# Kernel tuning notes

Measured on AMD Instinct MI355X. Metric: run time of the kernel, lower is better.

The kernel has to match this reference:

```python
import jax, jax.numpy as jnp
import numpy as np

N_NODES = 100000

def gin_conv(x, edge_index, W, b):
    # PyG GINConv with eps=0: out = Linear(x + sum_{j->i} x_j)
    src, dst = edge_index[0], edge_index[1]
    agg = jax.ops.segment_sum(x[src], dst, num_segments=N_NODES)  # [N, d]
    return (x + agg) @ W + b

def setup_inputs() -> dict:
    key = jax.random.key(0)
    ks = jax.random.split(key, 8)
    x = jax.random.normal(ks[0], (N_NODES, 32), dtype=jnp.float32)
    edge_index = jax.random.randint(ks[1], (2, 1600000), 0, N_NODES, dtype=jnp.int64)
    def lin(k, fan_in, fan_out):
        kw, kb = jax.random.split(k)
        lim = 1.0 / np.sqrt(fan_in)
        W = jax.random.uniform(kw, (fan_in, fan_out), minval=-lim, maxval=lim, dtype=jnp.float32)
        b = jax.random.uniform(kb, (fan_out,), minval=-lim, maxval=lim, dtype=jnp.float32)
        return W, b
    W1, b1 = lin(ks[2], 32, 64)
    W2, b2 = lin(ks[3], 64, 64)
    W3, b3 = lin(ks[4], 64, 10)
    return {"x": x, "edge_index": edge_index,
            "W1": W1, "b1": b1, "W2": W2, "b2": b2, "W3": W3, "b3": b3}

def reference(x, edge_index, W1, b1, W2, b2, W3, b3):
    h = jax.nn.relu(gin_conv(x, edge_index, W1, b1))
    h = jax.nn.relu(gin_conv(h, edge_index, W2, b2))
    return gin_conv(h, edge_index, W3, b3)  # [N, classes] logits
```

## Files before the change

### kernel.cpp

```cpp
#include <hip/hip_runtime.h>


#define GIN_N 100000
#define NBUCKET 256
#define NB2 391
#define BSTRIDE 8192
#define EPT 16

typedef float v2f __attribute__((ext_vector_type(2)));
typedef float f32x4 __attribute__((ext_vector_type(4)));
typedef short s16x8 __attribute__((ext_vector_type(8)));
typedef unsigned int u32x4 __attribute__((ext_vector_type(4)));

__device__ __forceinline__ float bf_lo(unsigned int u) {
    return __uint_as_float(u << 16);
}
__device__ __forceinline__ float bf_hi(unsigned int u) {
    return __uint_as_float(u & 0xffff0000u);
}
__device__ __forceinline__ unsigned int f2bf(float f) {
    unsigned int u = __float_as_uint(f);
    return (u + 0x7fffu + ((u >> 16) & 1u)) >> 16;
}
__device__ __forceinline__ unsigned pk2bf(float lo, float hi) {
    return f2bf(lo) | (f2bf(hi) << 16);
}
__device__ __forceinline__ v2f fp8lo(unsigned u) {
    return __builtin_amdgcn_cvt_pk_f32_fp8(u, false);
}
__device__ __forceinline__ v2f fp8hi(unsigned u) {
    return __builtin_amdgcn_cvt_pk_f32_fp8(u, true);
}
__device__ __forceinline__ s16x8 lds_frag(const unsigned* p) {
    return __builtin_bit_cast(s16x8, *reinterpret_cast<const u32x4*>(p));
}

template <int S>
__device__ __forceinline__ void blelloch_excl(int* a) {
#pragma unroll
    for (int d = 1; d < S; d <<= 1) {
        __syncthreads();
        int idx = (threadIdx.x + 1) * (d << 1) - 1;
        if (idx < S) a[idx] += a[idx - d];
    }
    __syncthreads();
    if (threadIdx.x == 0) a[S - 1] = 0;
#pragma unroll
    for (int d = S >> 1; d >= 1; d >>= 1) {
        __syncthreads();
        int idx = (threadIdx.x + 1) * (d << 1) - 1;
        if (idx < S) {
            int t = a[idx - d];
            a[idx - d] = a[idx];
            a[idx] += t;
        }
    }
    __syncthreads();
}

__global__ __launch_bounds__(256) void build_kernel(
        const int* __restrict__ src, const int* __restrict__ dst, int E,
        unsigned* __restrict__ bucketbuf, int* __restrict__ cursor,
        const float* __restrict__ x, unsigned* __restrict__ xq, int n8,
        int bblk) {
    __shared__ int h[NBUCKET];
    __shared__ int base[NBUCKET];
    int tid = threadIdx.x;
    if (blockIdx.x >= bblk) {
        int t = (blockIdx.x - bblk) * 256 + tid;
        if (t >= n8) return;
        const float4* v = reinterpret_cast<const float4*>(x);
        float4 a = v[2 * t], b = v[2 * t + 1];
        unsigned w0 = 0, w1 = 0;
        w0 = __builtin_amdgcn_cvt_pk_fp8_f32(a.x, a.y, w0, false);
        w0 = __builtin_amdgcn_cvt_pk_fp8_f32(a.z, a.w, w0, true);
        w1 = __builtin_amdgcn_cvt_pk_fp8_f32(b.x, b.y, w1, false);
        w1 = __builtin_amdgcn_cvt_pk_fp8_f32(b.z, b.w, w1, true);
        reinterpret_cast<uint2*>(xq)[t] = make_uint2(w0, w1);
        return;
    }
    int chunk0 = blockIdx.x * (256 * EPT);
    h[tid] = 0;
    __syncthreads();
    int myb[EPT];
    unsigned myrec[EPT];
#pragma unroll
    for (int i = 0; i < EPT; ++i) {
        int e = chunk0 + tid + i * 256;
        if (e < E) {
            int d = dst[e];
            int s = src[e];
            int b = d / NB2;
            myb[i] = b;
            myrec[i] = ((unsigned)(d - b * NB2) << 17) | (unsigned)s;
            atomicAdd(&h[b], 1);
        } else {
            myb[i] = -1;
        }
    }
    __syncthreads();
    base[tid] = atomicAdd(&cursor[tid], h[tid]);
    h[tid] = 0;
    __syncthreads();
#pragma unroll
    for (int i = 0; i < EPT; ++i) {
        int b = myb[i];
        if (b < 0) continue;
        int pos = base[b] + atomicAdd(&h[b], 1);
        if (pos < BSTRIDE) bucketbuf[(size_t)b * BSTRIDE + pos] = myrec[i];
    }
}

__global__ __launch_bounds__(256) void csr_build_kernel(
        const unsigned* __restrict__ bucketbuf,
        const int* __restrict__ cursor,
        int* __restrict__ rowptr,
        int* __restrict__ adj) {
    __shared__ int csr[BSTRIDE];
    __shared__ int cnt[512];
    __shared__ int off[512];
    __shared__ int bscan[NBUCKET];
    int b = blockIdx.x;
    int tid = threadIdx.x;
    bscan[tid] = cursor[tid];
    int mycnt = cursor[b];
    if (mycnt > BSTRIDE) mycnt = BSTRIDE;
    blelloch_excl<NBUCKET>(bscan);
    int base = bscan[b];

    const unsigned* buf = bucketbuf + (size_t)b * BSTRIDE;
    cnt[tid] = 0;
    cnt[tid + 256] = 0;
    __syncthreads();
    for (int i = tid; i < mycnt; i += 256)
        atomicAdd(&cnt[buf[i] >> 17], 1);
    __syncthreads();
    off[tid] = cnt[tid];
    off[tid + 256] = cnt[tid + 256];
    blelloch_excl<512>(off);

    int nodes0 = b * NB2;
    int nn2 = GIN_N + 1 - nodes0;
    if (nn2 > NB2) nn2 = NB2;
    for (int l = tid; l < nn2; l += 256) rowptr[nodes0 + l] = base + off[l];
    __syncthreads();

    for (int i = tid; i < mycnt; i += 256) {
        unsigned r = buf[i];
        int pos = atomicAdd(&off[r >> 17], 1);
        csr[pos] = (int)(r & 0x1FFFFu);
    }
    __syncthreads();
    for (int i = tid; i < mycnt; i += 256) adj[base + i] = csr[i];
}

__global__ __launch_bounds__(256, 8) void fused1_kernel(
        const float* __restrict__ xf,
        const unsigned* __restrict__ xq,
        const int* __restrict__ rowptr,
        const int* __restrict__ adj,
        const float* __restrict__ W,
        const float* __restrict__ b,
        unsigned* __restrict__ outq) {
    constexpr int K = 32, M = 64;
    constexpr int TPN = 4, NODES = 64;
    constexpr int KW = K / 2;
    constexpr int WSTR = KW + 4;

    __shared__ unsigned Wb[M * WSTR];
    __shared__ float bs[M];
    __shared__ unsigned tile[NODES * WSTR];

    int tid = threadIdx.x;
    for (int i = tid; i < M * KW; i += 256) {
        int k2 = i >> 6, j = i & 63;
        Wb[j * WSTR + k2] = pk2bf(W[(2 * k2) * M + j], W[(2 * k2 + 1) * M + j]);
    }
    if (tid < M) bs[tid] = b[tid];

    int node0 = blockIdx.x * NODES;

    {
        int l = tid / TPN;
        int j = tid % TPN;
        int n = node0 + l;
        if (n < GIN_N) {
            int start = rowptr[n];
            int d = rowptr[n + 1] - start;
            const int* row = adj + start;
            const uint2* fq = reinterpret_cast<const uint2*>(xq);
            v2f a0, a1, a2, a3;
            {
                const float4* xv = reinterpret_cast<const float4*>(xf);
                float4 a = xv[(size_t)n * 8 + 2 * j];
                float4 c = xv[(size_t)n * 8 + 2 * j + 1];
                a0 = v2f{a.x, a.y}; a1 = v2f{a.z, a.w};
                a2 = v2f{c.x, c.y}; a3 = v2f{c.z, c.w};
            }
#define ACC8(v) { a0 += fp8lo(v.x); a1 += fp8hi(v.x); \
                  a2 += fp8lo(v.y); a3 += fp8hi(v.y); }
            int k = 0;
            for (; k + 8 <= d; k += 8) {
                uint2 v0 = fq[(size_t)row[k] * 4 + j];
                uint2 v1 = fq[(size_t)row[k + 1] * 4 + j];
                uint2 v2 = fq[(size_t)row[k + 2] * 4 + j];
                uint2 v3 = fq[(size_t)row[k + 3] * 4 + j];
                uint2 v4 = fq[(size_t)row[k + 4] * 4 + j];
                uint2 v5 = fq[(size_t)row[k + 5] * 4 + j];
                uint2 v6 = fq[(size_t)row[k + 6] * 4 + j];
                uint2 v7 = fq[(size_t)row[k + 7] * 4 + j];
                ACC8(v0) ACC8(v1) ACC8(v2) ACC8(v3)
                ACC8(v4) ACC8(v5) ACC8(v6) ACC8(v7)
            }
            for (; k + 4 <= d; k += 4) {
                uint2 v0 = fq[(size_t)row[k] * 4 + j];
                uint2 v1 = fq[(size_t)row[k + 1] * 4 + j];
                uint2 v2 = fq[(size_t)row[k + 2] * 4 + j];
                uint2 v3 = fq[(size_t)row[k + 3] * 4 + j];
                ACC8(v0) ACC8(v1) ACC8(v2) ACC8(v3)
            }
            for (; k < d; ++k) {
                uint2 v = fq[(size_t)row[k] * 4 + j];
                ACC8(v)
            }
#undef ACC8
            *reinterpret_cast<uint4*>(&tile[l * WSTR + j * 4]) = make_uint4(
                pk2bf(a0.x, a0.y), pk2bf(a1.x, a1.y),
                pk2bf(a2.x, a2.y), pk2bf(a3.x, a3.y));
        }
    }
    __syncthreads();

    {
        int w = tid >> 6;
        int l = tid & 63;
        int c = l & 15;
        int g = l >> 4;
        int n = node0 + w * 16 + c;
        s16x8 bf = lds_frag(&tile[(w * 16 + c) * WSTR + 4 * g]);
#pragma unroll
        for (int jt = 0; jt < 4; ++jt) {
            int j0 = jt * 16;
            s16x8 af = lds_frag(&Wb[(j0 + c) * WSTR + 4 * g]);
            f32x4 a;
            a.x = bs[j0 + 4 * g + 0];
            a.y = bs[j0 + 4 * g + 1];
            a.z = bs[j0 + 4 * g + 2];
            a.w = bs[j0 + 4 * g + 3];
            a = __builtin_amdgcn_mfma_f32_16x16x32_bf16(af, bf, a, 0, 0, 0);
            float r0 = fmaxf(a.x, 0.0f), r1 = fmaxf(a.y, 0.0f);
            float r2 = fmaxf(a.z, 0.0f), r3 = fmaxf(a.w, 0.0f);
            unsigned u = 0;
            u = __builtin_amdgcn_cvt_pk_fp8_f32(r0, r1, u, false);
            u = __builtin_amdgcn_cvt_pk_fp8_f32(r2, r3, u, true);
            if (n < GIN_N) outq[(size_t)n * 16 + jt * 4 + g] = u;
        }
    }
}

__global__ __launch_bounds__(256, 8) void fused2t_kernel(
        const unsigned* __restrict__ xq,
        const int* __restrict__ rowptr,
        const int* __restrict__ adj,
        const float* __restrict__ W,
        const float* __restrict__ b,
        const float* __restrict__ W3,
        unsigned* __restrict__ tout) {
    constexpr int K = 64, M = 64;
    constexpr int TPN = 8, NODES = 32;
    constexpr int KW = K / 2;
    constexpr int WSTR = KW + 4;

    __shared__ unsigned Wb[M * WSTR];
    __shared__ float bs[M];
    __shared__ float W3n[M * 12];
    __shared__ unsigned tile[NODES * WSTR];
    __shared__ float ptb[2][NODES][10];

    int tid = threadIdx.x;
    for (int i = tid; i < M * KW; i += 256) {
        int k2 = i >> 6, j = i & 63;
        Wb[j * WSTR + k2] = pk2bf(W[(2 * k2) * M + j], W[(2 * k2 + 1) * M + j]);
    }
    for (int i = tid; i < M * 10; i += 256) {
        int j = i / 10, jj = i - 10 * j;
        W3n[j * 12 + jj] = W3[i];
    }
    if (tid < M) bs[tid] = b[tid];

    int node0 = blockIdx.x * NODES;

    {
        int l = tid / TPN;
        int j = tid % TPN;
        int n = node0 + l;
        if (n < GIN_N) {
            int start = rowptr[n];
            int d = rowptr[n + 1] - start;
            const int* row = adj + start;
            const uint2* fq = reinterpret_cast<const uint2*>(xq);
            v2f a0, a1, a2, a3;
            {
                uint2 s = fq[(size_t)n * 8 + j];
                a0 = fp8lo(s.x); a1 = fp8hi(s.x);
                a2 = fp8lo(s.y); a3 = fp8hi(s.y);
            }
#define ACC8(v) { a0 += fp8lo(v.x); a1 += fp8hi(v.x); \
                  a2 += fp8lo(v.y); a3 += fp8hi(v.y); }
            int k = 0;
            for (; k + 8 <= d; k += 8) {
                uint2 v0 = fq[(size_t)row[k] * 8 + j];
                uint2 v1 = fq[(size_t)row[k + 1] * 8 + j];
                uint2 v2 = fq[(size_t)row[k + 2] * 8 + j];
                uint2 v3 = fq[(size_t)row[k + 3] * 8 + j];
                uint2 v4 = fq[(size_t)row[k + 4] * 8 + j];
                uint2 v5 = fq[(size_t)row[k + 5] * 8 + j];
                uint2 v6 = fq[(size_t)row[k + 6] * 8 + j];
                uint2 v7 = fq[(size_t)row[k + 7] * 8 + j];
                ACC8(v0) ACC8(v1) ACC8(v2) ACC8(v3)
                ACC8(v4) ACC8(v5) ACC8(v6) ACC8(v7)
            }
            for (; k + 4 <= d; k += 4) {
                uint2 v0 = fq[(size_t)row[k] * 8 + j];
                uint2 v1 = fq[(size_t)row[k + 1] * 8 + j];
                uint2 v2 = fq[(size_t)row[k + 2] * 8 + j];
                uint2 v3 = fq[(size_t)row[k + 3] * 8 + j];
                ACC8(v0) ACC8(v1) ACC8(v2) ACC8(v3)
            }
            for (; k < d; ++k) {
                uint2 v = fq[(size_t)row[k] * 8 + j];
                ACC8(v)
            }
#undef ACC8
            *reinterpret_cast<uint4*>(&tile[l * WSTR + j * 4]) = make_uint4(
                pk2bf(a0.x, a0.y), pk2bf(a1.x, a1.y),
                pk2bf(a2.x, a2.y), pk2bf(a3.x, a3.y));
        }
    }
    __syncthreads();

    {
        int w  = tid >> 6;
        int l  = tid & 63;
        int c  = l & 15;
        int g  = l >> 4;
        int nt = w & 1;
        int jp = w >> 1;
        const unsigned* trow = &tile[(nt * 16 + c) * WSTR];
        s16x8 bf0 = lds_frag(trow + 4 * g);
        s16x8 bf1 = lds_frag(trow + 16 + 4 * g);
        f32x4 acc[2];
#pragma unroll
        for (int jt = 0; jt < 2; ++jt) {
            int j0 = (2 * jp + jt) * 16;
            const unsigned* arow = &Wb[(j0 + c) * WSTR];
            s16x8 af0 = lds_frag(arow + 4 * g);
            s16x8 af1 = lds_frag(arow + 16 + 4 * g);
            f32x4 a;
            a.x = bs[j0 + 4 * g + 0];
            a.y = bs[j0 + 4 * g + 1];
            a.z = bs[j0 + 4 * g + 2];
            a.w = bs[j0 + 4 * g + 3];
            a = __builtin_amdgcn_mfma_f32_16x16x32_bf16(af0, bf0, a, 0, 0, 0);
            a = __builtin_amdgcn_mfma_f32_16x16x32_bf16(af1, bf1, a, 0, 0, 0);
            acc[jt] = a;
        }
        v2f pt[5];
#pragma unroll
        for (int q = 0; q < 5; ++q) pt[q] = v2f{0.0f, 0.0f};
#pragma unroll
        for (int jt = 0; jt < 2; ++jt) {
            int jb = (2 * jp + jt) * 16 + 4 * g;
#pragma unroll
            for (int r = 0; r < 4; ++r) {
                float h = fmaxf(acc[jt][r], 0.0f);
                const v2f* wr =
                    reinterpret_cast<const v2f*>(&W3n[(jb + r) * 12]);
#pragma unroll
                for (int q = 0; q < 5; ++q) pt[q] += wr[q] * h;
            }
        }
        float ptf[10];
#pragma unroll
        for (int q = 0; q < 5; ++q) { ptf[2 * q] = pt[q].x; ptf[2 * q + 1] = pt[q].y; }
#pragma unroll
        for (int jj = 0; jj < 10; ++jj) {
            float v = ptf[jj];
            v += __shfl_xor(v, 16, 64);
            v += __shfl_xor(v, 32, 64);
            ptf[jj] = v;
        }
        if (g == 0) {
#pragma unroll
            for (int jj = 0; jj < 10; ++jj)
                ptb[jp][nt * 16 + c][jj] = ptf[jj];
        }
    }
    __syncthreads();

    {
        int n = tid >> 3, q = tid & 7;
        int node = node0 + n;
        unsigned u = 0;
        if (q < 5) {
            float lo = ptb[0][n][2 * q]     + ptb[1][n][2 * q];
            float hi = ptb[0][n][2 * q + 1] + ptb[1][n][2 * q + 1];
            u = pk2bf(lo, hi);
        }
        if (node < GIN_N) tout[(size_t)node * 8 + q] = u;
    }
}

__global__ void gather_final_kernel(const unsigned* __restrict__ t8,
                                    const int* __restrict__ rowptr,
                                    const int* __restrict__ adj,
                                    const float* __restrict__ b3,
                                    float* __restrict__ out) {
    int t = blockIdx.x * blockDim.x + threadIdx.x;
    int n = t >> 3;
    int j = t & 7;
    if (n >= GIN_N || j >= 5) return;
    int start = rowptr[n];
    int d = rowptr[n + 1] - start;
    const int* row = adj + start;
    unsigned sv = t8[(size_t)n * 8 + j];
    float a0 = bf_lo(sv), a1 = bf_hi(sv);
    int k = 0;
    for (; k + 4 <= d; k += 4) {
        int r0 = row[k], r1 = row[k + 1], r2 = row[k + 2], r3 = row[k + 3];
        unsigned v0 = t8[(size_t)r0 * 8 + j];
        unsigned v1 = t8[(size_t)r1 * 8 + j];
        unsigned v2 = t8[(size_t)r2 * 8 + j];
        unsigned v3 = t8[(size_t)r3 * 8 + j];
        a0 += bf_lo(v0) + bf_lo(v1) + bf_lo(v2) + bf_lo(v3);
        a1 += bf_hi(v0) + bf_hi(v1) + bf_hi(v2) + bf_hi(v3);
    }
    for (; k < d; ++k) {
        unsigned v = t8[(size_t)row[k] * 8 + j];
        a0 += bf_lo(v); a1 += bf_hi(v);
    }
    out[(size_t)n * 10 + 2 * j] = a0 + b3[2 * j];
    out[(size_t)n * 10 + 2 * j + 1] = a1 + b3[2 * j + 1];
}

extern "C" void kernel_launch(void* const* d_in, const int* in_sizes, int n_in,
                              void* d_out, int out_size, void* d_ws, size_t ws_size,
                              hipStream_t stream) {
    const float* x  = (const float*)d_in[0];
    const int*   ei = (const int*)d_in[1];
    const float* W1 = (const float*)d_in[2];
    const float* b1 = (const float*)d_in[3];
    const float* W2 = (const float*)d_in[4];
    const float* b2 = (const float*)d_in[5];
    const float* W3 = (const float*)d_in[6];
    const float* b3 = (const float*)d_in[7];
    float* out = (float*)d_out;

    const int N = GIN_N;
    const int E = in_sizes[1] / 2;
    const int* src = ei;
    const int* dst = ei + E;

    unsigned* Xq = (unsigned*)d_ws;
    unsigned* H1q = Xq + (size_t)N * 8;
    unsigned* Tb = H1q + (size_t)N * 16;
    int* rowptr = (int*)(Tb + (size_t)N * 8);
    int* cursor = rowptr + (N + 8);
    int* adj = cursor + 256;
    unsigned* bucketbuf = (unsigned*)(adj + (size_t)E);

    const int BLK = 256;

    hipMemsetAsync(cursor, 0, 256 * sizeof(int), stream);
    {
        int n8 = N * 32 / 8;
        int bblk = (E + BLK * EPT - 1) / (BLK * EPT);
        int xblk = (n8 + BLK - 1) / BLK;
        build_kernel<<<bblk + xblk, BLK, 0, stream>>>(
            src, dst, E, bucketbuf, cursor, x, Xq, n8, bblk);
        csr_build_kernel<<<NBUCKET, BLK, 0, stream>>>(
            bucketbuf, cursor, rowptr, adj);
    }

    fused1_kernel<<<(N + 63) / 64, BLK, 0, stream>>>(
        x, Xq, rowptr, adj, W1, b1, H1q);

    fused2t_kernel<<<(N + 31) / 32, BLK, 0, stream>>>(
        H1q, rowptr, adj, W2, b2, W3, Tb);

    gather_final_kernel<<<(N * 8 + BLK - 1) / BLK, BLK, 0, stream>>>(
        Tb, rowptr, adj, b3, out);
}
```

Measured before the change: 186.8 us.

## Pad CSR rows to multiples of four with dummy node for int4 neighbor loads

Each CSR row is padded to a multiple of four entries. The padding points to a zeroed dummy node N appended to every feature buffer, and a separate degree array is added. All three gather kernels now read neighbor indices as int4 vectors with no scalar tail loops. The build kernel also reuses the first-pass atomic rank instead of doing a second atomic pass, and the final gather packs 5 threads per node with float2 stores instead of leaving 3 of 8 lanes idle. In exchange the adjacency array grows, up to three extra dummy gathers are done per node, and zeroing the padding nodes needs extra memsets.

```diff
diff --git a/kernel.cpp b/kernel.cpp
--- a/kernel.cpp
+++ b/kernel.cpp
@@ -82,7 +82,7 @@
     int chunk0 = blockIdx.x * (256 * EPT);
     h[tid] = 0;
     __syncthreads();
-    int myb[EPT];
+    unsigned mybr[EPT];
     unsigned myrec[EPT];
 #pragma unroll
     for (int i = 0; i < EPT; ++i) {
@@ -91,22 +91,21 @@
             int d = dst[e];
             int s = src[e];
             int b = d / NB2;
-            myb[i] = b;
+            int rank = atomicAdd(&h[b], 1);
+            mybr[i] = ((unsigned)rank << 8) | (unsigned)b;
             myrec[i] = ((unsigned)(d - b * NB2) << 17) | (unsigned)s;
-            atomicAdd(&h[b], 1);
         } else {
-            myb[i] = -1;
+            mybr[i] = 0xFFFFFFFFu;
         }
     }
     __syncthreads();
     base[tid] = atomicAdd(&cursor[tid], h[tid]);
-    h[tid] = 0;
     __syncthreads();
 #pragma unroll
     for (int i = 0; i < EPT; ++i) {
-        int b = myb[i];
-        if (b < 0) continue;
-        int pos = base[b] + atomicAdd(&h[b], 1);
+        if (mybr[i] == 0xFFFFFFFFu) continue;
+        int b = (int)(mybr[i] & 0xFFu);
+        int pos = base[b] + (int)(mybr[i] >> 8);
         if (pos < BSTRIDE) bucketbuf[(size_t)b * BSTRIDE + pos] = myrec[i];
     }
 }
@@ -115,14 +114,20 @@
         const unsigned* __restrict__ bucketbuf,
         const int* __restrict__ cursor,
         int* __restrict__ rowptr,
+        int* __restrict__ deg,
         int* __restrict__ adj) {
     __shared__ int csr[BSTRIDE];
     __shared__ int cnt[512];
     __shared__ int off[512];
     __shared__ int bscan[NBUCKET];
+    __shared__ int tot;
     int b = blockIdx.x;
     int tid = threadIdx.x;
-    bscan[tid] = cursor[tid];
+    {
+        int c = cursor[tid];
+        if (c > BSTRIDE) c = BSTRIDE;
+        bscan[tid] = (c + 3 * NB2 + 3) & ~3;
+    }
     int mycnt = cursor[b];
     if (mycnt > BSTRIDE) mycnt = BSTRIDE;
     blelloch_excl<NBUCKET>(bscan);
@@ -135,29 +140,42 @@
     for (int i = tid; i < mycnt; i += 256)
         atomicAdd(&cnt[buf[i] >> 17], 1);
     __syncthreads();
-    off[tid] = cnt[tid];
-    off[tid + 256] = cnt[tid + 256];
+    off[tid] = (cnt[tid] + 3) & ~3;
+    off[tid + 256] = (cnt[tid + 256] + 3) & ~3;
     blelloch_excl<512>(off);
+    if (tid == 0) tot = off[511] + ((cnt[511] + 3) & ~3);
 
     int nodes0 = b * NB2;
     int nn2 = GIN_N + 1 - nodes0;
     if (nn2 > NB2) nn2 = NB2;
+    int nnode = GIN_N - nodes0;
+    if (nnode > NB2) nnode = NB2;
     for (int l = tid; l < nn2; l += 256) rowptr[nodes0 + l] = base + off[l];
+    for (int l = tid; l < nnode; l += 256) {
+        deg[nodes0 + l] = cnt[l];
+        int s = off[l] + cnt[l];
+        int e2 = off[l] + ((cnt[l] + 3) & ~3);
+        for (int p = s; p < e2; ++p)
+            if (p < BSTRIDE) csr[p] = GIN_N;
+    }
     __syncthreads();
 
     for (int i = tid; i < mycnt; i += 256) {
         unsigned r = buf[i];
         int pos = atomicAdd(&off[r >> 17], 1);
-        csr[pos] = (int)(r & 0x1FFFFu);
-    }
-    __syncthreads();
-    for (int i = tid; i < mycnt; i += 256) adj[base + i] = csr[i];
+        if (pos < BSTRIDE) csr[pos] = (int)(r & 0x1FFFFu);
+    }
+    __syncthreads();
+    int T = tot;
+    if (T > BSTRIDE) T = BSTRIDE;
+    for (int i = tid; i < T; i += 256) adj[base + i] = csr[i];
 }
 
 __global__ __launch_bounds__(256, 8) void fused1_kernel(
         const float* __restrict__ xf,
         const unsigned* __restrict__ xq,
         const int* __restrict__ rowptr,
+        const int* __restrict__ deg,
         const int* __restrict__ adj,
         const float* __restrict__ W,
         const float* __restrict__ b,
@@ -186,8 +204,8 @@
         int n = node0 + l;
         if (n < GIN_N) {
             int start = rowptr[n];
-            int d = rowptr[n + 1] - start;
-            const int* row = adj + start;
+            int n4 = (deg[n] + 3) >> 2;
+            const int4* row4 = reinterpret_cast<const int4*>(adj + start);
             const uint2* fq = reinterpret_cast<const uint2*>(xq);
             v2f a0, a1, a2, a3;
             {
@@ -199,29 +217,27 @@
             }
 #define ACC8(v) { a0 += fp8lo(v.x); a1 += fp8hi(v.x); \
                   a2 += fp8lo(v.y); a3 += fp8hi(v.y); }
-            int k = 0;
-            for (; k + 8 <= d; k += 8) {
-                uint2 v0 = fq[(size_t)row[k] * 4 + j];
-                uint2 v1 = fq[(size_t)row[k + 1] * 4 + j];
-                uint2 v2 = fq[(size_t)row[k + 2] * 4 + j];
-                uint2 v3 = fq[(size_t)row[k + 3] * 4 + j];
-                uint2 v4 = fq[(size_t)row[k + 4] * 4 + j];
-                uint2 v5 = fq[(size_t)row[k + 5] * 4 + j];
-                uint2 v6 = fq[(size_t)row[k + 6] * 4 + j];
-                uint2 v7 = fq[(size_t)row[k + 7] * 4 + j];
+            int q = 0;
+            for (; q + 2 <= n4; q += 2) {
+                int4 ra = row4[q], rb = row4[q + 1];
+                uint2 v0 = fq[(size_t)ra.x * 4 + j];
+                uint2 v1 = fq[(size_t)ra.y * 4 + j];
+                uint2 v2 = fq[(size_t)ra.z * 4 + j];
+                uint2 v3 = fq[(size_t)ra.w * 4 + j];
+                uint2 v4 = fq[(size_t)rb.x * 4 + j];
+                uint2 v5 = fq[(size_t)rb.y * 4 + j];
+                uint2 v6 = fq[(size_t)rb.z * 4 + j];
+                uint2 v7 = fq[(size_t)rb.w * 4 + j];
                 ACC8(v0) ACC8(v1) ACC8(v2) ACC8(v3)
                 ACC8(v4) ACC8(v5) ACC8(v6) ACC8(v7)
             }
-            for (; k + 4 <= d; k += 4) {
-                uint2 v0 = fq[(size_t)row[k] * 4 + j];
-                uint2 v1 = fq[(size_t)row[k + 1] * 4 + j];
-                uint2 v2 = fq[(size_t)row[k + 2] * 4 + j];
-                uint2 v3 = fq[(size_t)row[k + 3] * 4 + j];
+            if (q < n4) {
+                int4 ra = row4[q];
+                uint2 v0 = fq[(size_t)ra.x * 4 + j];
+                uint2 v1 = fq[(size_t)ra.y * 4 + j];
+                uint2 v2 = fq[(size_t)ra.z * 4 + j];
+                uint2 v3 = fq[(size_t)ra.w * 4 + j];
                 ACC8(v0) ACC8(v1) ACC8(v2) ACC8(v3)
-            }
-            for (; k < d; ++k) {
-                uint2 v = fq[(size_t)row[k] * 4 + j];
-                ACC8(v)
             }
 #undef ACC8
             *reinterpret_cast<uint4*>(&tile[l * WSTR + j * 4]) = make_uint4(
@@ -261,6 +277,7 @@
 __global__ __launch_bounds__(256, 8) void fused2t_kernel(
         const unsigned* __restrict__ xq,
         const int* __restrict__ rowptr,
+        const int* __restrict__ deg,
         const int* __restrict__ adj,
         const float* __restrict__ W,
         const float* __restrict__ b,
@@ -296,8 +313,8 @@
         int n = node0 + l;
         if (n < GIN_N) {
             int start = rowptr[n];
-            int d = rowptr[n + 1] - start;
-            const int* row = adj + start;
+            int n4 = (deg[n] + 3) >> 2;
+            const int4* row4 = reinterpret_cast<const int4*>(adj + start);
             const uint2* fq = reinterpret_cast<const uint2*>(xq);
             v2f a0, a1, a2, a3;
             {
@@ -307,29 +324,27 @@
             }
 #define ACC8(v) { a0 += fp8lo(v.x); a1 += fp8hi(v.x); \
                   a2 += fp8lo(v.y); a3 += fp8hi(v.y); }
-            int k = 0;
-            for (; k + 8 <= d; k += 8) {
-                uint2 v0 = fq[(size_t)row[k] * 8 + j];
-                uint2 v1 = fq[(size_t)row[k + 1] * 8 + j];
-                uint2 v2 = fq[(size_t)row[k + 2] * 8 + j];
-                uint2 v3 = fq[(size_t)row[k + 3] * 8 + j];
-                uint2 v4 = fq[(size_t)row[k + 4] * 8 + j];
-                uint2 v5 = fq[(size_t)row[k + 5] * 8 + j];
-                uint2 v6 = fq[(size_t)row[k + 6] * 8 + j];
-                uint2 v7 = fq[(size_t)row[k + 7] * 8 + j];
+            int q = 0;
+            for (; q + 2 <= n4; q += 2) {
+                int4 ra = row4[q], rb = row4[q + 1];
+                uint2 v0 = fq[(size_t)ra.x * 8 + j];
+                uint2 v1 = fq[(size_t)ra.y * 8 + j];
+                uint2 v2 = fq[(size_t)ra.z * 8 + j];
+                uint2 v3 = fq[(size_t)ra.w * 8 + j];
+                uint2 v4 = fq[(size_t)rb.x * 8 + j];
+                uint2 v5 = fq[(size_t)rb.y * 8 + j];
+                uint2 v6 = fq[(size_t)rb.z * 8 + j];
+                uint2 v7 = fq[(size_t)rb.w * 8 + j];
                 ACC8(v0) ACC8(v1) ACC8(v2) ACC8(v3)
                 ACC8(v4) ACC8(v5) ACC8(v6) ACC8(v7)
             }
-            for (; k + 4 <= d; k += 4) {
-                uint2 v0 = fq[(size_t)row[k] * 8 + j];
-                uint2 v1 = fq[(size_t)row[k + 1] * 8 + j];
-                uint2 v2 = fq[(size_t)row[k + 2] * 8 + j];
-                uint2 v3 = fq[(size_t)row[k + 3] * 8 + j];
+            if (q < n4) {
+                int4 ra = row4[q];
+                uint2 v0 = fq[(size_t)ra.x * 8 + j];
+                uint2 v1 = fq[(size_t)ra.y * 8 + j];
+                uint2 v2 = fq[(size_t)ra.z * 8 + j];
+                uint2 v3 = fq[(size_t)ra.w * 8 + j];
                 ACC8(v0) ACC8(v1) ACC8(v2) ACC8(v3)
-            }
-            for (; k < d; ++k) {
-                uint2 v = fq[(size_t)row[k] * 8 + j];
-                ACC8(v)
             }
 #undef ACC8
             *reinterpret_cast<uint4*>(&tile[l * WSTR + j * 4]) = make_uint4(
@@ -411,36 +426,51 @@
     }
 }
 
-__global__ void gather_final_kernel(const unsigned* __restrict__ t8,
-                                    const int* __restrict__ rowptr,
-                                    const int* __restrict__ adj,
-                                    const float* __restrict__ b3,
-                                    float* __restrict__ out) {
+__global__ __launch_bounds__(256) void gather_final_kernel(
+        const unsigned* __restrict__ t8,
+        const int* __restrict__ rowptr,
+        const int* __restrict__ deg,
+        const int* __restrict__ adj,
+        const float* __restrict__ b3,
+        float* __restrict__ out) {
     int t = blockIdx.x * blockDim.x + threadIdx.x;
-    int n = t >> 3;
-    int j = t & 7;
-    if (n >= GIN_N || j >= 5) return;
+    int n = t / 5;
+    int j = t - n * 5;
+    if (n >= GIN_N) return;
     int start = rowptr[n];
-    int d = rowptr[n + 1] - start;
-    const int* row = adj + start;
+    int n4 = (deg[n] + 3) >> 2;
+    const int4* row4 = reinterpret_cast<const int4*>(adj + start);
     unsigned sv = t8[(size_t)n * 8 + j];
     float a0 = bf_lo(sv), a1 = bf_hi(sv);
-    int k = 0;
-    for (; k + 4 <= d; k += 4) {
-        int r0 = row[k], r1 = row[k + 1], r2 = row[k + 2], r3 = row[k + 3];
-        unsigned v0 = t8[(size_t)r0 * 8 + j];
-        unsigned v1 = t8[(size_t)r1 * 8 + j];
-        unsigned v2 = t8[(size_t)r2 * 8 + j];
-        unsigned v3 = t8[(size_t)r3 * 8 + j];
+    int q = 0;
+    for (; q + 2 <= n4; q += 2) {
+        int4 ra = row4[q], rb = row4[q + 1];
+        unsigned v0 = t8[(size_t)ra.x * 8 + j];
+        unsigned v1 = t8[(size_t)ra.y * 8 + j];
+        unsigned v2 = t8[(size_t)ra.z * 8 + j];
+        unsigned v3 = t8[(size_t)ra.w * 8 + j];
+        unsigned v4 = t8[(size_t)rb.x * 8 + j];
+        unsigned v5 = t8[(size_t)rb.y * 8 + j];
+        unsigned v6 = t8[(size_t)rb.z * 8 + j];
+        unsigned v7 = t8[(size_t)rb.w * 8 + j];
         a0 += bf_lo(v0) + bf_lo(v1) + bf_lo(v2) + bf_lo(v3);
         a1 += bf_hi(v0) + bf_hi(v1) + bf_hi(v2) + bf_hi(v3);
-    }
-    for (; k < d; ++k) {
-        unsigned v = t8[(size_t)row[k] * 8 + j];
-        a0 += bf_lo(v); a1 += bf_hi(v);
-    }
-    out[(size_t)n * 10 + 2 * j] = a0 + b3[2 * j];
-    out[(size_t)n * 10 + 2 * j + 1] = a1 + b3[2 * j + 1];
+        a0 += bf_lo(v4) + bf_lo(v5) + bf_lo(v6) + bf_lo(v7);
+        a1 += bf_hi(v4) + bf_hi(v5) + bf_hi(v6) + bf_hi(v7);
+    }
+    if (q < n4) {
+        int4 ra = row4[q];
+        unsigned v0 = t8[(size_t)ra.x * 8 + j];
+        unsigned v1 = t8[(size_t)ra.y * 8 + j];
+        unsigned v2 = t8[(size_t)ra.z * 8 + j];
+        unsigned v3 = t8[(size_t)ra.w * 8 + j];
+        a0 += bf_lo(v0) + bf_lo(v1) + bf_lo(v2) + bf_lo(v3);
+        a1 += bf_hi(v0) + bf_hi(v1) + bf_hi(v2) + bf_hi(v3);
+    }
+    const float2* b2v = reinterpret_cast<const float2*>(b3);
+    float2 bb = b2v[j];
+    float2 r; r.x = a0 + bb.x; r.y = a1 + bb.y;
+    *reinterpret_cast<float2*>(out + (size_t)n * 10 + 2 * j) = r;
 }
 
 extern "C" void kernel_launch(void* const* d_in, const int* in_sizes, int n_in,
@@ -462,16 +492,21 @@
     const int* dst = ei + E;
 
     unsigned* Xq = (unsigned*)d_ws;
-    unsigned* H1q = Xq + (size_t)N * 8;
-    unsigned* Tb = H1q + (size_t)N * 16;
-    int* rowptr = (int*)(Tb + (size_t)N * 8);
-    int* cursor = rowptr + (N + 8);
+    unsigned* H1q = Xq + (size_t)(N + 1) * 8;
+    unsigned* Tb = H1q + (size_t)(N + 1) * 16;
+    int* rowptr = (int*)(Tb + (size_t)(N + 1) * 8);
+    int* deg = rowptr + (N + 8);
+    int* cursor = deg + (N + 8);
     int* adj = cursor + 256;
-    unsigned* bucketbuf = (unsigned*)(adj + (size_t)E);
+    unsigned* bucketbuf = (unsigned*)(adj + (size_t)E + 256 * (3 * NB2 + 4));
 
     const int BLK = 256;
 
     hipMemsetAsync(cursor, 0, 256 * sizeof(int), stream);
+    hipMemsetAsync(Xq + (size_t)N * 8, 0, 32, stream);
+    hipMemsetAsync(H1q + (size_t)N * 16, 0, 64, stream);
+    hipMemsetAsync(Tb + (size_t)N * 8, 0, 32, stream);
+
     {
         int n8 = N * 32 / 8;
         int bblk = (E + BLK * EPT - 1) / (BLK * EPT);
@@ -479,15 +514,15 @@
         build_kernel<<<bblk + xblk, BLK, 0, stream>>>(
             src, dst, E, bucketbuf, cursor, x, Xq, n8, bblk);
         csr_build_kernel<<<NBUCKET, BLK, 0, stream>>>(
-            bucketbuf, cursor, rowptr, adj);
+            bucketbuf, cursor, rowptr, deg, adj);
     }
 
     fused1_kernel<<<(N + 63) / 64, BLK, 0, stream>>>(
-        x, Xq, rowptr, adj, W1, b1, H1q);
+        x, Xq, rowptr, deg, adj, W1, b1, H1q);
 
     fused2t_kernel<<<(N + 31) / 32, BLK, 0, stream>>>(
-        H1q, rowptr, adj, W2, b2, W3, Tb);
-
-    gather_final_kernel<<<(N * 8 + BLK - 1) / BLK, BLK, 0, stream>>>(
-        Tb, rowptr, adj, b3, out);
-}
+        H1q, rowptr, deg, adj, W2, b2, W3, Tb);
+
+    gather_final_kernel<<<(N * 5 + BLK - 1) / BLK, BLK, 0, stream>>>(
+        Tb, rowptr, deg, adj, b3, out);
+}
```

Measured after the change: 195.9 us. 1.05x slower.
